# Optimization experiments

Measured on AMD Instinct MI355X. Metric: run time of the kernel, lower is better.

## Reference

```python
import jax, jax.numpy as jnp
import numpy as np

DIM = 1024
HEADS = 16
SEQ = 1024
N_EXP = 2
SLOTS = SEQ // N_EXP  # slots per expert; total slots == seq_len as in SoftMoE(dim, seq_len, num_experts)
HID = 4 * DIM         # expert FFN hidden
EPS = 1e-5


def layernorm(x, g, b):
    mu = x.mean(-1, keepdims=True)
    var = x.var(-1, keepdims=True)
    return (x - mu) * jax.lax.rsqrt(var + EPS) * g + b


def setup_inputs() -> dict:
    key = jax.random.key(0)
    ks = jax.random.split(key, 16)
    s = lambda k, shape, scale=0.02: jax.random.normal(k, shape, jnp.float32) * scale
    return {
        "x": jax.random.normal(ks[0], (4, SEQ, DIM), jnp.float32),
        "Wq": s(ks[1], (DIM, DIM)), "bq": jnp.zeros((DIM,), jnp.float32),
        "Wkv": s(ks[2], (DIM, 2 * DIM)), "bkv": jnp.zeros((2 * DIM,), jnp.float32),
        "Wp": s(ks[3], (DIM, DIM)), "bp": jnp.zeros((DIM,), jnp.float32),
        "g1": jnp.ones((DIM,), jnp.float32), "b1": jnp.zeros((DIM,), jnp.float32),
        "phi": s(ks[4], (DIM, N_EXP, SLOTS)),
        "We1": s(ks[5], (N_EXP, DIM, HID)), "be1": jnp.zeros((N_EXP, HID), jnp.float32),
        "We2": s(ks[6], (N_EXP, HID, DIM)), "be2": jnp.zeros((N_EXP, DIM), jnp.float32),
        "g2": jnp.ones((DIM,), jnp.float32), "b2": jnp.zeros((DIM,), jnp.float32),
    }


def soft_moe(x, phi, We1, be1, We2, be2):
    # x: [b,n,d]; phi: [d,e,s]
    logits = jnp.einsum("bnd,des->bnes", x, phi)
    dispatch = jax.nn.softmax(logits, axis=1)                    # over sequence
    b, n, e, s = logits.shape
    combine = jax.nn.softmax(logits.reshape(b, n, e * s), axis=-1).reshape(b, n, e, s)
    slots = jnp.einsum("bnd,bnes->besd", x, dispatch)            # [b,e,s,d]
    h = jax.nn.gelu(jnp.einsum("besd,edh->besh", slots, We1) + be1[None, :, None, :])
    y = jnp.einsum("besh,ehd->besd", h, We2) + be2[None, :, None, :]
    return jnp.einsum("besd,bnes->bnd", y, combine)


def reference(x, Wq, bq, Wkv, bkv, Wp, bp, g1, b1, phi, We1, be1, We2, be2, g2, b2):
    b, n, c = x.shape
    hd = c // HEADS
    scale = hd ** -0.5
    q = (x @ Wq + bq).reshape(b, n, HEADS, hd)
    kv = (x @ Wkv + bkv).reshape(b, n, 2, HEADS, hd)
    k, v = kv[:, :, 0], kv[:, :, 1]
    attn = jnp.einsum("bnhd,bmhd->bnmh", q, k) * scale
    attn = jax.nn.softmax(attn, axis=2)
    out = jnp.einsum("bnmh,bmhd->bnhd", attn, v).reshape(b, n, c)
    out = out @ Wp + bp
    x1 = layernorm(out + x, g1, b1)
    x2 = x1 + soft_moe(x1, phi, We1, be1, We2, be2)
    y = layernorm(x2 + x1, g2, b2)
    return (y, attn)
```

## Files before the change

kernel.cpp:

```cpp
#include <hip/hip_runtime.h>
#include <math.h>

#define BATCH 4
#define SEQ   1024
#define DIM   1024
#define HEADS 16
#define HD    64
#define NEXP  2
#define NSLOT 512
#define ES    1024
#define HID   4096
#define LNEPS 1e-5f
#define NTOK  (BATCH*SEQ)

typedef long long ll;
typedef unsigned short ushort;
typedef unsigned int uint;
typedef __attribute__((ext_vector_type(8))) short short8;
typedef __attribute__((ext_vector_type(4))) float f32x4;
typedef __attribute__((ext_vector_type(4))) unsigned short us4;

__device__ __forceinline__ ushort f2b(float f) {
    uint u = __builtin_bit_cast(uint, f);
    u += 0x7FFFu + ((u >> 16) & 1u);
    return (ushort)(u >> 16);
}
__device__ __forceinline__ float b2f(ushort h) {
    uint u = ((uint)h) << 16;
    return __builtin_bit_cast(float, u);
}
__device__ __forceinline__ uint pk(float a, float b) {
    return (uint)f2b(a) | ((uint)f2b(b) << 16);
}
__device__ __forceinline__ float gelu_f(float v) {
    float x3 = v * v * v;
    return 0.5f * v * (1.f + tanhf(0.7978845608028654f * (v + 0.044715f * x3)));
}

__device__ __forceinline__ void gload16(const ushort* g, ushort* l) {
    __builtin_amdgcn_global_load_lds(
        (const __attribute__((address_space(1))) unsigned int*)(const void*)g,
        (__attribute__((address_space(3))) unsigned int*)(void*)l,
        16, 0, 0);
}

__global__ __launch_bounds__(256) void cvt_bf16(
    const float* __restrict__ src, ushort* __restrict__ dst)
{
    int i = blockIdx.x * 256 + threadIdx.x;
    const float4* s = reinterpret_cast<const float4*>(src) + (ll)i * 2;
    float4 a = s[0], b = s[1];
    uint4 w;
    w.x = pk(a.x, a.y); w.y = pk(a.z, a.w);
    w.z = pk(b.x, b.y); w.w = pk(b.z, b.w);
    reinterpret_cast<uint4*>(dst)[i] = w;
}

__global__ __launch_bounds__(256) void concat_bias(
    const float* __restrict__ a, const float* __restrict__ b,
    float* __restrict__ o)
{
    int i = blockIdx.x * 256 + threadIdx.x;
    o[i] = (i < DIM) ? a[i] : b[i - DIM];
}

template<typename TS>
__global__ __launch_bounds__(256) void transpose_cvt(
    const TS* __restrict__ src, int ldsrc, ll sS1, ll sS2,
    ushort* __restrict__ dst, int lddst, ll sD1, ll sD2, int Z2)
{
    __shared__ ushort tile[64][68];
    const int z1 = blockIdx.z / Z2, z2 = blockIdx.z % Z2;
    src += z1 * sS1 + z2 * sS2;
    dst += z1 * sD1 + z2 * sD2;
    const int r0 = blockIdx.y * 64, c0 = blockIdx.x * 64;
    const int t = threadIdx.x;
    #pragma unroll
    for (int j = 0; j < 4; j++) {
        int idx = t + 256 * j;
        int r = idx >> 4, c = (idx & 15) * 4;
        if constexpr (sizeof(TS) == 4) {
            float4 v = *reinterpret_cast<const float4*>(src + (ll)(r0 + r) * ldsrc + c0 + c);
            tile[r][c]     = f2b(v.x);
            tile[r][c + 1] = f2b(v.y);
            tile[r][c + 2] = f2b(v.z);
            tile[r][c + 3] = f2b(v.w);
        } else {
            *reinterpret_cast<us4*>(&tile[r][c]) =
                *reinterpret_cast<const us4*>(src + (ll)(r0 + r) * ldsrc + c0 + c);
        }
    }
    __syncthreads();
    #pragma unroll
    for (int j = 0; j < 4; j++) {
        int idx = t + 256 * j;
        int rr = idx >> 4, cc = (idx & 15) * 4;
        us4 w;
        w.x = tile[cc][rr]; w.y = tile[cc + 1][rr];
        w.z = tile[cc + 2][rr]; w.w = tile[cc + 3][rr];
        *reinterpret_cast<us4*>(&dst[(ll)(c0 + rr) * lddst + r0 + cc]) = w;
    }
}

template<int WR, int WC, int MI, int NI, int ACT, typename TC>
__global__ __launch_bounds__(256) void gemm_bf16(
    const ushort* __restrict__ A, int lda, ll sA1, ll sA2,
    const ushort* __restrict__ B, int ldb, ll sB1, ll sB2,
    const float* __restrict__ bias, ll sb1, ll sb2,
    TC* __restrict__ C, int ldc, ll sC1, ll sC2,
    int K, int Z2, float alpha)
{
    constexpr int BM = WR * MI * 16;
    constexpr int BN = WC * NI * 16;
    __shared__ alignas(16) ushort As[BM * 32];
    __shared__ alignas(16) ushort Bs[BN * 32];

    const int z1 = blockIdx.z / Z2, z2 = blockIdx.z % Z2;
    A += z1 * sA1 + z2 * sA2;
    B += z1 * sB1 + z2 * sB2;
    C += z1 * sC1 + z2 * sC2;

    const int t = threadIdx.x;
    const int m0 = blockIdx.y * BM, n0 = blockIdx.x * BN;
    const int lane = t & 63, wave = t >> 6;
    const int quad = lane >> 4, l16 = lane & 15;
    const int wm = wave / WC, wn = wave % WC;

    f32x4 acc[MI][NI] = {};

    for (int k0 = 0; k0 < K; k0 += 32) {
        #pragma unroll
        for (int i = 0; i < BM / 64; i++) {
            int seg = i * 256 + t;
            int row = seg >> 2, ke = (seg & 3) * 8;
            gload16(A + (ll)(m0 + row) * lda + (k0 + ke), &As[seg * 8]);
        }
        #pragma unroll
        for (int i = 0; i < BN / 64; i++) {
            int seg = i * 256 + t;
            int row = seg >> 2, ke = (seg & 3) * 8;
            gload16(B + (ll)(n0 + row) * ldb + (k0 + ke), &Bs[seg * 8]);
        }
        __syncthreads();

        short8 a[MI], b[NI];
        #pragma unroll
        for (int mi = 0; mi < MI; mi++)
            a[mi] = *reinterpret_cast<const short8*>(
                &As[(wm * MI * 16 + mi * 16 + l16) * 32 + quad * 8]);
        #pragma unroll
        for (int ni = 0; ni < NI; ni++)
            b[ni] = *reinterpret_cast<const short8*>(
                &Bs[(wn * NI * 16 + ni * 16 + l16) * 32 + quad * 8]);
        #pragma unroll
        for (int mi = 0; mi < MI; mi++)
            #pragma unroll
            for (int ni = 0; ni < NI; ni++)
                acc[mi][ni] = __builtin_amdgcn_mfma_f32_16x16x32_bf16(
                    a[mi], b[ni], acc[mi][ni], 0, 0, 0);
        __syncthreads();
    }

    const float* bz = bias ? (bias + z1 * sb1 + z2 * sb2) : nullptr;
    #pragma unroll
    for (int mi = 0; mi < MI; mi++) {
        #pragma unroll
        for (int ni = 0; ni < NI; ni++) {
            const int row = m0 + wm * MI * 16 + mi * 16 + quad * 4;
            const int col = n0 + wn * NI * 16 + ni * 16 + l16;
            const float bv = bz ? bz[col] : 0.f;
            #pragma unroll
            for (int r = 0; r < 4; r++) {
                float v = alpha * acc[mi][ni][r] + bv;
                if (ACT) v = gelu_f(v);
                if constexpr (sizeof(TC) == 2)
                    C[(ll)(row + r) * ldc + col] = f2b(v);
                else
                    C[(ll)(row + r) * ldc + col] = v;
            }
        }
    }
}

__global__ __launch_bounds__(256) void attn_softmax(
    ushort* __restrict__ p, float* __restrict__ attn_out)
{
    __shared__ float tile[16][1024];
    const int n = blockIdx.x, b = blockIdx.y;
    const int t = threadIdx.x;
    const int lane = t & 63, w = t >> 6;
    ushort* base = p + ((ll)(b * SEQ + n) * HEADS) * SEQ;
    #pragma unroll 1
    for (int g = 0; g < 4; g++) {
        const int h = g * 4 + w;
        ushort* row = base + (ll)h * SEQ + lane * 16;
        uint4 r0 = reinterpret_cast<const uint4*>(row)[0];
        uint4 r1 = reinterpret_cast<const uint4*>(row)[1];
        uint rr[8] = {r0.x, r0.y, r0.z, r0.w, r1.x, r1.y, r1.z, r1.w};
        float v[16];
        float m = -3.0e38f;
        #pragma unroll
        for (int j = 0; j < 8; j++) {
            v[2 * j]     = b2f((ushort)(rr[j] & 0xFFFFu));
            v[2 * j + 1] = b2f((ushort)(rr[j] >> 16));
            m = fmaxf(m, fmaxf(v[2 * j], v[2 * j + 1]));
        }
        #pragma unroll
        for (int o = 32; o; o >>= 1) m = fmaxf(m, __shfl_xor(m, o));
        float s = 0.f;
        #pragma unroll
        for (int j = 0; j < 16; j++) { v[j] = __expf(v[j] - m); s += v[j]; }
        #pragma unroll
        for (int o = 32; o; o >>= 1) s += __shfl_xor(s, o);
        const float inv = 1.f / s;
        #pragma unroll
        for (int j = 0; j < 16; j++) v[j] *= inv;
        uint pw[8];
        #pragma unroll
        for (int j = 0; j < 8; j++) pw[j] = pk(v[2 * j], v[2 * j + 1]);
        uint4 w0, w1;
        w0.x = pw[0]; w0.y = pw[1]; w0.z = pw[2]; w0.w = pw[3];
        w1.x = pw[4]; w1.y = pw[5]; w1.z = pw[6]; w1.w = pw[7];
        reinterpret_cast<uint4*>(row)[0] = w0;
        reinterpret_cast<uint4*>(row)[1] = w1;
        #pragma unroll
        for (int jj = 0; jj < 4; jj++) {
            float4 f4;
            f4.x = v[4 * jj]; f4.y = v[4 * jj + 1];
            f4.z = v[4 * jj + 2]; f4.w = v[4 * jj + 3];
            *reinterpret_cast<float4*>(&tile[h][(jj * 64 + lane) * 4]) = f4;
        }
    }
    __syncthreads();
    float* outp = attn_out + ((ll)b * SEQ + n) * SEQ * HEADS;
    #pragma unroll
    for (int jj = 0; jj < 4; jj++) {
        const int mm = t + 256 * jj;
        const int gm = mm >> 2;
        const int fi = ((gm & 3) * 64 + (gm >> 2)) * 4 + (mm & 3);
        float o16[16];
        #pragma unroll
        for (int h = 0; h < 16; h++) o16[h] = tile[h][fi];
        float4* dst = reinterpret_cast<float4*>(outp + (ll)mm * HEADS);
        #pragma unroll
        for (int q = 0; q < 4; q++) {
            float4 o4;
            o4.x = o16[4 * q]; o4.y = o16[4 * q + 1];
            o4.z = o16[4 * q + 2]; o4.w = o16[4 * q + 3];
            dst[q] = o4;
        }
    }
}

__global__ __launch_bounds__(256) void ln_kernel(
    const float* __restrict__ a, const float* __restrict__ b, float coef,
    const float* __restrict__ g, const float* __restrict__ beta,
    float* __restrict__ out, ushort* __restrict__ out_bf)
{
    const int row = blockIdx.x;
    const int t = threadIdx.x;
    float4 av = reinterpret_cast<const float4*>(a + (ll)row * DIM)[t];
    float4 bv = reinterpret_cast<const float4*>(b + (ll)row * DIM)[t];
    float4 v;
    v.x = av.x + coef * bv.x; v.y = av.y + coef * bv.y;
    v.z = av.z + coef * bv.z; v.w = av.w + coef * bv.w;
    float s1 = v.x + v.y + v.z + v.w;
    float s2 = v.x * v.x + v.y * v.y + v.z * v.z + v.w * v.w;
    __shared__ float red[8];
    #pragma unroll
    for (int o = 32; o; o >>= 1) { s1 += __shfl_xor(s1, o); s2 += __shfl_xor(s2, o); }
    int w = t >> 6;
    if ((t & 63) == 0) { red[w] = s1; red[4 + w] = s2; }
    __syncthreads();
    s1 = red[0] + red[1] + red[2] + red[3];
    s2 = red[4] + red[5] + red[6] + red[7];
    float mu = s1 * (1.f / DIM);
    float var = s2 * (1.f / DIM) - mu * mu;
    float rs = rsqrtf(var + LNEPS);
    float4 gv = reinterpret_cast<const float4*>(g)[t];
    float4 be = reinterpret_cast<const float4*>(beta)[t];
    float4 o;
    o.x = (v.x - mu) * rs * gv.x + be.x;
    o.y = (v.y - mu) * rs * gv.y + be.y;
    o.z = (v.z - mu) * rs * gv.z + be.z;
    o.w = (v.w - mu) * rs * gv.w + be.w;
    reinterpret_cast<float4*>(out + (ll)row * DIM)[t] = o;
    if (out_bf) {
        us4 hv;
        hv.x = f2b(o.x); hv.y = f2b(o.y); hv.z = f2b(o.z); hv.w = f2b(o.w);
        reinterpret_cast<us4*>(out_bf + (ll)row * DIM)[t] = hv;
    }
}

__global__ __launch_bounds__(256) void col_softmax(
    const float* __restrict__ logits, ushort* __restrict__ dispT)
{
    const int b = blockIdx.x, cc = blockIdx.y;
    const int cl = threadIdx.x & 63;
    const int c = cc * 64 + cl;
    const int rg = threadIdx.x >> 6;
    const float* L = logits + (ll)b * SEQ * ES + c;
    ushort* DT = dispT + (ll)b * ES * SEQ + (ll)c * SEQ;
    __shared__ float red[4][64];
    float m = -3.0e38f;
    for (int n = rg; n < SEQ; n += 4) m = fmaxf(m, L[(ll)n * ES]);
    red[rg][cl] = m;
    __syncthreads();
    m = fmaxf(fmaxf(red[0][cl], red[1][cl]), fmaxf(red[2][cl], red[3][cl]));
    __syncthreads();
    float s = 0.f;
    for (int n = rg; n < SEQ; n += 4) s += __expf(L[(ll)n * ES] - m);
    red[rg][cl] = s;
    __syncthreads();
    s = red[0][cl] + red[1][cl] + red[2][cl] + red[3][cl];
    float inv = 1.f / s;
    for (int n = rg; n < SEQ; n += 4)
        DT[n] = f2b(__expf(L[(ll)n * ES] - m) * inv);
}

__global__ __launch_bounds__(256) void row_softmax(
    const float* __restrict__ logits, ushort* __restrict__ comb)
{
    const int row = blockIdx.x;
    const float* L = logits + (ll)row * ES;
    ushort* O = comb + (ll)row * ES;
    float v[4];
    float m = -3.0e38f;
    #pragma unroll
    for (int j = 0; j < 4; j++) { v[j] = L[threadIdx.x + 256 * j]; m = fmaxf(m, v[j]); }
    __shared__ float red[8];
    #pragma unroll
    for (int o = 32; o; o >>= 1) m = fmaxf(m, __shfl_xor(m, o));
    int w = threadIdx.x >> 6;
    if ((threadIdx.x & 63) == 0) red[w] = m;
    __syncthreads();
    m = fmaxf(fmaxf(red[0], red[1]), fmaxf(red[2], red[3]));
    __syncthreads();
    float s = 0.f;
    #pragma unroll
    for (int j = 0; j < 4; j++) { v[j] = __expf(v[j] - m); s += v[j]; }
    #pragma unroll
    for (int o = 32; o; o >>= 1) s += __shfl_xor(s, o);
    if ((threadIdx.x & 63) == 0) red[4 + w] = s;
    __syncthreads();
    s = red[4] + red[5] + red[6] + red[7];
    float inv = 1.f / s;
    #pragma unroll
    for (int j = 0; j < 4; j++) O[threadIdx.x + 256 * j] = f2b(v[j] * inv);
}

extern "C" void kernel_launch(void* const* d_in, const int* in_sizes, int n_in,
                              void* d_out, int out_size, void* d_ws, size_t ws_size,
                              hipStream_t stream)
{
    const float* x   = (const float*)d_in[0];
    const float* Wq  = (const float*)d_in[1];
    const float* bq  = (const float*)d_in[2];
    const float* Wkv = (const float*)d_in[3];
    const float* bkv = (const float*)d_in[4];
    const float* Wp  = (const float*)d_in[5];
    const float* bp  = (const float*)d_in[6];
    const float* g1  = (const float*)d_in[7];
    const float* b1  = (const float*)d_in[8];
    const float* phi = (const float*)d_in[9];
    const float* We1 = (const float*)d_in[10];
    const float* be1 = (const float*)d_in[11];
    const float* We2 = (const float*)d_in[12];
    const float* be2 = (const float*)d_in[13];
    const float* g2  = (const float*)d_in[14];
    const float* b2  = (const float*)d_in[15];

    float* out_y    = (float*)d_out;
    float* out_attn = out_y + (ll)BATCH * SEQ * DIM;

    const ll M1 = 1024 * 1024;
    float*  ws     = (float*)d_ws;
    ushort* x_bf   = (ushort*)(ws);
    ushort* WqkvT  = (ushort*)(ws + 2 * M1);
    ushort* WpT    = (ushort*)(ws + 7 * M1 / 2);
    ushort* phiT   = (ushort*)(ws + 4 * M1);
    ushort* qkv_bf = (ushort*)(ws + 9 * M1 / 2);
    ushort* vT     = (ushort*)(ws + 21 * M1 / 2);
    ushort* p_bf   = (ushort*)(ws + 25 * M1 / 2);
    float*  po     = ws + 25 * M1 / 2;
    ushort* ao_bf  = (ushort*)(ws + 89 * M1 / 2);
    ushort* ymoeT  = (ushort*)(ws + 89 * M1 / 2);
    float*  x1     = ws + 33 * M1 / 2;
    ushort* x1_bf  = (ushort*)(ws + 41 * M1 / 2);
    ushort* x1T    = (ushort*)(ws + 45 * M1 / 2);
    float*  logit  = ws + 49 * M1 / 2;
    ushort* dispT  = (ushort*)(ws + 57 * M1 / 2);
    ushort* comb   = (ushort*)(ws + 61 * M1 / 2);
    ushort* slots  = (ushort*)(ws + 65 * M1 / 2);
    ushort* hmid   = (ushort*)(ws + 69 * M1 / 2);
    ushort* ymoe   = (ushort*)(ws + 85 * M1 / 2);
    ushort* We1T   = (ushort*)(ws + 9 * M1 / 2);
    ushort* We2T   = (ushort*)(ws + 17 * M1 / 2);
    float*  bqkv   = ws + 93 * M1 / 2;
    float*  moe    = ws;

    dim3 blk(256);

    cvt_bf16<<<dim3(2048), blk, 0, stream>>>(x, x_bf);
    transpose_cvt<float><<<dim3(16, 16, 1), blk, 0, stream>>>(
        Wq, DIM, 0, 0, WqkvT, DIM, 0, 0, 1);
    transpose_cvt<float><<<dim3(32, 16, 1), blk, 0, stream>>>(
        Wkv, 2 * DIM, 0, 0, WqkvT + (ll)DIM * DIM, DIM, 0, 0, 1);
    transpose_cvt<float><<<dim3(16, 16, 1), blk, 0, stream>>>(
        Wp, DIM, 0, 0, WpT, DIM, 0, 0, 1);
    transpose_cvt<float><<<dim3(16, 16, 1), blk, 0, stream>>>(
        phi, ES, 0, 0, phiT, DIM, 0, 0, 1);
    concat_bias<<<dim3(12), blk, 0, stream>>>(bq, bkv, bqkv);

    gemm_bf16<2,2,4,4,0,ushort><<<dim3(24, 32, 1), blk, 0, stream>>>(
        x_bf, DIM, 0, 0, WqkvT, DIM, 0, 0, bqkv, 0, 0,
        qkv_bf, 3 * DIM, 0, 0, DIM, 1, 1.f);

    transpose_cvt<ushort><<<dim3(1, 16, BATCH * HEADS), blk, 0, stream>>>(
        qkv_bf + 2 * DIM, 3 * DIM, (ll)SEQ * 3 * DIM, HD,
        vT, SEQ, (ll)HEADS * HD * SEQ, (ll)HD * SEQ, HEADS);

    gemm_bf16<2,2,4,4,0,ushort><<<dim3(8, 8, BATCH * HEADS), blk, 0, stream>>>(
        qkv_bf, 3 * DIM, (ll)SEQ * 3 * DIM, HD,
        qkv_bf + DIM, 3 * DIM, (ll)SEQ * 3 * DIM, HD,
        nullptr, 0, 0,
        p_bf, HEADS * SEQ, (ll)SEQ * HEADS * SEQ, (ll)SEQ,
        HD, HEADS, 0.125f);

    attn_softmax<<<dim3(SEQ, BATCH), blk, 0, stream>>>(p_bf, out_attn);

    gemm_bf16<4,1,2,4,0,ushort><<<dim3(1, 8, BATCH * HEADS), blk, 0, stream>>>(
        p_bf, HEADS * SEQ, (ll)SEQ * HEADS * SEQ, (ll)SEQ,
        vT, SEQ, (ll)HEADS * HD * SEQ, (ll)HD * SEQ,
        nullptr, 0, 0,
        ao_bf, DIM, (ll)SEQ * DIM, HD,
        SEQ, HEADS, 1.f);

    gemm_bf16<2,2,4,4,0,float><<<dim3(8, 32, 1), blk, 0, stream>>>(
        ao_bf, DIM, 0, 0, WpT, DIM, 0, 0, bp, 0, 0,
        po, DIM, 0, 0, DIM, 1, 1.f);
    ln_kernel<<<dim3(NTOK), blk, 0, stream>>>(po, x, 1.0f, g1, b1, x1, x1_bf);

    transpose_cvt<float><<<dim3(64, 16, 2), blk, 0, stream>>>(
        We1, HID, 0, (ll)DIM * HID, We1T, DIM, 0, (ll)HID * DIM, 2);
    transpose_cvt<float><<<dim3(16, 64, 2), blk, 0, stream>>>(
        We2, DIM, 0, (ll)HID * DIM, We2T, HID, 0, (ll)DIM * HID, 2);
    transpose_cvt<ushort><<<dim3(16, 16, BATCH), blk, 0, stream>>>(
        x1_bf, DIM, (ll)SEQ * DIM, 0, x1T, SEQ, (ll)DIM * SEQ, 0, 1);

    gemm_bf16<2,2,4,4,0,float><<<dim3(8, 32, 1), blk, 0, stream>>>(
        x1_bf, DIM, 0, 0, phiT, DIM, 0, 0, nullptr, 0, 0,
        logit, ES, 0, 0, DIM, 1, 1.f);
    col_softmax<<<dim3(BATCH, 16), blk, 0, stream>>>(logit, dispT);
    row_softmax<<<dim3(NTOK), blk, 0, stream>>>(logit, comb);

    gemm_bf16<2,2,4,4,0,ushort><<<dim3(8, 8, BATCH), blk, 0, stream>>>(
        dispT, SEQ, (ll)ES * SEQ, 0,
        x1T, SEQ, (ll)DIM * SEQ, 0,
        nullptr, 0, 0,
        slots, DIM, (ll)ES * DIM, 0,
        SEQ, 1, 1.f);

    gemm_bf16<2,2,4,4,1,ushort><<<dim3(32, 4, BATCH * NEXP), blk, 0, stream>>>(
        slots, DIM, (ll)ES * DIM, (ll)NSLOT * DIM,
        We1T, DIM, 0, (ll)HID * DIM,
        be1, 0, HID,
        hmid, HID, (ll)ES * HID, (ll)NSLOT * HID,
        DIM, NEXP, 1.f);

    gemm_bf16<2,2,4,4,0,ushort><<<dim3(8, 4, BATCH * NEXP), blk, 0, stream>>>(
        hmid, HID, (ll)ES * HID, (ll)NSLOT * HID,
        We2T, HID, 0, (ll)DIM * HID,
        be2, 0, DIM,
        ymoe, DIM, (ll)ES * DIM, (ll)NSLOT * DIM,
        HID, NEXP, 1.f);

    transpose_cvt<ushort><<<dim3(16, 16, BATCH), blk, 0, stream>>>(
        ymoe, DIM, (ll)ES * DIM, 0, ymoeT, ES, (ll)DIM * ES, 0, 1);

    gemm_bf16<2,2,4,4,0,float><<<dim3(8, 8, BATCH), blk, 0, stream>>>(
        comb, ES, (ll)SEQ * ES, 0,
        ymoeT, ES, (ll)DIM * ES, 0,
        nullptr, 0, 0,
        moe, DIM, (ll)SEQ * DIM, 0,
        ES, 1, 1.f);

    ln_kernel<<<dim3(NTOK), blk, 0, stream>>>(moe, x1, 2.0f, g2, b2, out_y, nullptr);
}
```

Before: 1.065 ms.

## Add triple-buffered 512-thread GEMM with split MFMA phases for dense projections

Introduces a new GEMM kernel using 512 threads, BK=64 tiles, a three-stage LDS ring with direct global-to-LDS loads, and interleaved staging of the next tiles between two MFMA half-phases with raised wave priority. Most dense GEMMs (QKV, output projection, router logits, slot dispatch, expert FFNs, combine) move to it with larger tiles. The aim is to hide global memory latency and raise MFMA utilisation. In exchange it uses much more LDS per block (up to about 147KB for 256x128), which limits occupancy, and the larger tiles shrink the grid for the smaller GEMMs.

Measured after the change: 1.003 ms. -5.8%, faster.

```diff
diff --git a/kernel.cpp b/kernel.cpp
--- a/kernel.cpp
+++ b/kernel.cpp
@@ -167,6 +167,147 @@
         #pragma unroll
         for (int ni = 0; ni < NI; ni++) {
             const int row = m0 + wm * MI * 16 + mi * 16 + quad * 4;
+            const int col = n0 + wn * NI * 16 + ni * 16 + l16;
+            const float bv = bz ? bz[col] : 0.f;
+            #pragma unroll
+            for (int r = 0; r < 4; r++) {
+                float v = alpha * acc[mi][ni][r] + bv;
+                if (ACT) v = gelu_f(v);
+                if constexpr (sizeof(TC) == 2)
+                    C[(ll)(row + r) * ldc + col] = f2b(v);
+                else
+                    C[(ll)(row + r) * ldc + col] = v;
+            }
+        }
+    }
+}
+
+template<int BM, int BN, int ACT, typename TC>
+__global__ __launch_bounds__(512) void gemm2(
+    const ushort* __restrict__ A, int lda, ll sA1, ll sA2,
+    const ushort* __restrict__ B, int ldb, ll sB1, ll sB2,
+    const float* __restrict__ bias, ll sb1, ll sb2,
+    TC* __restrict__ C, int ldc, ll sC1, ll sC2,
+    int K, int Z2, float alpha)
+{
+    constexpr int WR = BM / 64;
+    constexpr int WC = 8 / WR;
+    constexpr int MI = 4;
+    constexpr int NI = BN / WC / 16;
+    constexpr int NH = NI / 2 ? NI / 2 : 1;
+    constexpr int LA = BM / 64;
+    constexpr int LB = BN / 64;
+
+    __shared__ alignas(16) ushort As[3][BM * 64];
+    __shared__ alignas(16) ushort Bs[3][BN * 64];
+
+    const int z1 = blockIdx.z / Z2, z2 = blockIdx.z % Z2;
+    A += z1 * sA1 + z2 * sA2;
+    B += z1 * sB1 + z2 * sB2;
+    C += z1 * sC1 + z2 * sC2;
+
+    const int t = threadIdx.x;
+    const int lane = t & 63, wave = t >> 6;
+    const int quad = lane >> 4, l16 = lane & 15;
+    const int wm = wave / WC, wn = wave % WC;
+    const int m0 = blockIdx.y * BM, n0 = blockIdx.x * BN;
+
+    auto stageA = [&](int kt) {
+        const ushort* src = A + (ll)m0 * lda + kt * 64;
+        ushort* dst = As[kt % 3];
+        #pragma unroll
+        for (int j = 0; j < LA; j++) {
+            int seg = j * 512 + t;
+            int row = seg >> 3, kk = (seg & 7) * 8;
+            gload16(src + (ll)row * lda + kk, dst + seg * 8);
+        }
+    };
+    auto stageB = [&](int kt) {
+        const ushort* src = B + (ll)n0 * ldb + kt * 64;
+        ushort* dst = Bs[kt % 3];
+        #pragma unroll
+        for (int j = 0; j < LB; j++) {
+            int seg = j * 512 + t;
+            int row = seg >> 3, kk = (seg & 7) * 8;
+            gload16(src + (ll)row * ldb + kk, dst + seg * 8);
+        }
+    };
+
+    f32x4 acc[MI][NI] = {};
+    const int NK = K / 64;
+
+    stageA(0); stageB(0);
+    if (NK > 1) { stageA(1); stageB(1); }
+
+    for (int kt = 0; kt < NK; kt++) {
+        if (kt + 1 < NK)
+            asm volatile("s_waitcnt vmcnt(%0)" :: "n"(LA + LB) : "memory");
+        else
+            asm volatile("s_waitcnt vmcnt(0)" ::: "memory");
+        __builtin_amdgcn_sched_barrier(0);
+        __builtin_amdgcn_s_barrier();
+        __builtin_amdgcn_sched_barrier(0);
+
+        const ushort* Abuf = As[kt % 3];
+        const ushort* Bbuf = Bs[kt % 3];
+
+        short8 a[MI][2], b0[NH][2];
+        #pragma unroll
+        for (int mi = 0; mi < MI; mi++)
+            #pragma unroll
+            for (int kh = 0; kh < 2; kh++)
+                a[mi][kh] = *reinterpret_cast<const short8*>(
+                    &Abuf[(wm * 64 + mi * 16 + l16) * 64 + kh * 32 + quad * 8]);
+        #pragma unroll
+        for (int ni = 0; ni < NH; ni++)
+            #pragma unroll
+            for (int kh = 0; kh < 2; kh++)
+                b0[ni][kh] = *reinterpret_cast<const short8*>(
+                    &Bbuf[(wn * NI * 16 + ni * 16 + l16) * 64 + kh * 32 + quad * 8]);
+        if (kt + 2 < NK) stageA(kt + 2);
+        asm volatile("s_waitcnt lgkmcnt(0)" ::: "memory");
+        __builtin_amdgcn_sched_barrier(0);
+        __builtin_amdgcn_s_setprio(1);
+        #pragma unroll
+        for (int mi = 0; mi < MI; mi++)
+            #pragma unroll
+            for (int ni = 0; ni < NH; ni++)
+                #pragma unroll
+                for (int kh = 0; kh < 2; kh++)
+                    acc[mi][ni] = __builtin_amdgcn_mfma_f32_16x16x32_bf16(
+                        a[mi][kh], b0[ni][kh], acc[mi][ni], 0, 0, 0);
+        __builtin_amdgcn_s_setprio(0);
+        __builtin_amdgcn_sched_barrier(0);
+
+        short8 b1[NH][2];
+        #pragma unroll
+        for (int ni = 0; ni < NH; ni++)
+            #pragma unroll
+            for (int kh = 0; kh < 2; kh++)
+                b1[ni][kh] = *reinterpret_cast<const short8*>(
+                    &Bbuf[(wn * NI * 16 + (NH + ni) * 16 + l16) * 64 + kh * 32 + quad * 8]);
+        if (kt + 2 < NK) stageB(kt + 2);
+        asm volatile("s_waitcnt lgkmcnt(0)" ::: "memory");
+        __builtin_amdgcn_sched_barrier(0);
+        __builtin_amdgcn_s_setprio(1);
+        #pragma unroll
+        for (int mi = 0; mi < MI; mi++)
+            #pragma unroll
+            for (int ni = 0; ni < NH; ni++)
+                #pragma unroll
+                for (int kh = 0; kh < 2; kh++)
+                    acc[mi][NH + ni] = __builtin_amdgcn_mfma_f32_16x16x32_bf16(
+                        a[mi][kh], b1[ni][kh], acc[mi][NH + ni], 0, 0, 0);
+        __builtin_amdgcn_s_setprio(0);
+        __builtin_amdgcn_sched_barrier(0);
+    }
+
+    const float* bz = bias ? (bias + z1 * sb1 + z2 * sb2) : nullptr;
+    #pragma unroll
+    for (int mi = 0; mi < MI; mi++) {
+        #pragma unroll
+        for (int ni = 0; ni < NI; ni++) {
+            const int row = m0 + wm * 64 + mi * 16 + quad * 4;
             const int col = n0 + wn * NI * 16 + ni * 16 + l16;
             const float bv = bz ? bz[col] : 0.f;
             #pragma unroll
@@ -399,7 +540,7 @@
     float*  bqkv   = ws + 93 * M1 / 2;
     float*  moe    = ws;
 
-    dim3 blk(256);
+    dim3 blk(256), blk5(512);
 
     cvt_bf16<<<dim3(2048), blk, 0, stream>>>(x, x_bf);
     transpose_cvt<float><<<dim3(16, 16, 1), blk, 0, stream>>>(
@@ -412,7 +553,7 @@
         phi, ES, 0, 0, phiT, DIM, 0, 0, 1);
     concat_bias<<<dim3(12), blk, 0, stream>>>(bq, bkv, bqkv);
 
-    gemm_bf16<2,2,4,4,0,ushort><<<dim3(24, 32, 1), blk, 0, stream>>>(
+    gemm2<256,128,0,ushort><<<dim3(24, 16, 1), blk5, 0, stream>>>(
         x_bf, DIM, 0, 0, WqkvT, DIM, 0, 0, bqkv, 0, 0,
         qkv_bf, 3 * DIM, 0, 0, DIM, 1, 1.f);
 
@@ -436,7 +577,7 @@
         ao_bf, DIM, (ll)SEQ * DIM, HD,
         SEQ, HEADS, 1.f);
 
-    gemm_bf16<2,2,4,4,0,float><<<dim3(8, 32, 1), blk, 0, stream>>>(
+    gemm2<128,128,0,float><<<dim3(8, 32, 1), blk5, 0, stream>>>(
         ao_bf, DIM, 0, 0, WpT, DIM, 0, 0, bp, 0, 0,
         po, DIM, 0, 0, DIM, 1, 1.f);
     ln_kernel<<<dim3(NTOK), blk, 0, stream>>>(po, x, 1.0f, g1, b1, x1, x1_bf);
@@ -448,27 +589,27 @@
     transpose_cvt<ushort><<<dim3(16, 16, BATCH), blk, 0, stream>>>(
         x1_bf, DIM, (ll)SEQ * DIM, 0, x1T, SEQ, (ll)DIM * SEQ, 0, 1);
 
-    gemm_bf16<2,2,4,4,0,float><<<dim3(8, 32, 1), blk, 0, stream>>>(
+    gemm2<128,128,0,float><<<dim3(8, 32, 1), blk5, 0, stream>>>(
         x1_bf, DIM, 0, 0, phiT, DIM, 0, 0, nullptr, 0, 0,
         logit, ES, 0, 0, DIM, 1, 1.f);
     col_softmax<<<dim3(BATCH, 16), blk, 0, stream>>>(logit, dispT);
     row_softmax<<<dim3(NTOK), blk, 0, stream>>>(logit, comb);
 
-    gemm_bf16<2,2,4,4,0,ushort><<<dim3(8, 8, BATCH), blk, 0, stream>>>(
+    gemm2<128,128,0,ushort><<<dim3(8, 8, BATCH), blk5, 0, stream>>>(
         dispT, SEQ, (ll)ES * SEQ, 0,
         x1T, SEQ, (ll)DIM * SEQ, 0,
         nullptr, 0, 0,
         slots, DIM, (ll)ES * DIM, 0,
         SEQ, 1, 1.f);
 
-    gemm_bf16<2,2,4,4,1,ushort><<<dim3(32, 4, BATCH * NEXP), blk, 0, stream>>>(
+    gemm2<256,128,1,ushort><<<dim3(32, 2, BATCH * NEXP), blk5, 0, stream>>>(
         slots, DIM, (ll)ES * DIM, (ll)NSLOT * DIM,
         We1T, DIM, 0, (ll)HID * DIM,
         be1, 0, HID,
         hmid, HID, (ll)ES * HID, (ll)NSLOT * HID,
         DIM, NEXP, 1.f);
 
-    gemm_bf16<2,2,4,4,0,ushort><<<dim3(8, 4, BATCH * NEXP), blk, 0, stream>>>(
+    gemm2<128,128,0,ushort><<<dim3(8, 4, BATCH * NEXP), blk5, 0, stream>>>(
         hmid, HID, (ll)ES * HID, (ll)NSLOT * HID,
         We2T, HID, 0, (ll)DIM * HID,
         be2, 0, DIM,
@@ -478,7 +619,7 @@
     transpose_cvt<ushort><<<dim3(16, 16, BATCH), blk, 0, stream>>>(
         ymoe, DIM, (ll)ES * DIM, 0, ymoeT, ES, (ll)DIM * ES, 0, 1);
 
-    gemm_bf16<2,2,4,4,0,float><<<dim3(8, 8, BATCH), blk, 0, stream>>>(
+    gemm2<128,128,0,float><<<dim3(8, 8, BATCH), blk5, 0, stream>>>(
         comb, ES, (ll)SEQ * ES, 0,
         ymoeT, ES, (ll)DIM * ES, 0,
         nullptr, 0, 0,
```
